# Kernel tuning notes

Hardware: AMD Instinct MI355X
Metric: run time of the kernel (lower is better)

The kernel has to match this reference:

```python
import jax, jax.numpy as jnp
import numpy as np
from jax import lax

EPS = 1e-5
ODE_T1 = 6.0      # ODEnet uses timestep=6
ODE_NSTEPS = 12   # fixed-step RK4 replacing scipy LSODA


def _gn(x, groups, w, b):
    # GroupNorm over (C//groups, H, W) per group, affine per-channel
    N, C, H, W = x.shape
    xg = x.reshape(N, groups, -1)
    mu = xg.mean(-1, keepdims=True)
    var = xg.var(-1, keepdims=True)
    xn = ((xg - mu) * lax.rsqrt(var + EPS)).reshape(N, C, H, W)
    return xn * w[None, :, None, None] + b[None, :, None, None]


def _conv(x, w, stride=1, pad=1):
    return lax.conv_general_dilated(
        x, w, (stride, stride), [(pad, pad), (pad, pad)],
        dimension_numbers=('NCHW', 'OIHW', 'NCHW'))


def _residual(x, g1w, g1b, c1w, g2w, g2b, c2w, dw):
    # Residual block with stride-2 conv and 1x1 stride-2 downsample applied
    # to relu(norm1(x)) (exactly as in the torch code).
    h = jax.nn.relu(_gn(x, 32, g1w, g1b))
    skip = _conv(h, dw, stride=2, pad=0)
    h = _conv(h, c1w, stride=2, pad=1)
    h = jax.nn.relu(_gn(h, 32, g2w, g2b))
    h = _conv(h, c2w)
    return h + skip


def _odefunc(z, p):
    # ResidualODE.odefunc: GroupNorm with groups == channels (64)
    g1w, g1b, c1w, g2w, g2b, c2w = p
    h = jax.nn.relu(_gn(z, 64, g1w, g1b))
    h = _conv(h, c1w)
    h = jax.nn.relu(_gn(h, 64, g2w, g2b))
    h = _conv(h, c2w)
    return h + z


def _odeint_rk4(z0, p):
    dt = ODE_T1 / ODE_NSTEPS
    def step(z, _):
        k1 = _odefunc(z, p)
        k2 = _odefunc(z + 0.5 * dt * k1, p)
        k3 = _odefunc(z + 0.5 * dt * k2, p)
        k4 = _odefunc(z + dt * k3, p)
        return z + (dt / 6.0) * (k1 + 2.0 * k2 + 2.0 * k3 + k4), None
    z, _ = lax.scan(step, z0, None, length=ODE_NSTEPS)
    return z


def _forward(x, conv1_w, conv1_b,
             r1_g1w, r1_g1b, r1_c1w, r1_g2w, r1_g2b, r1_c2w, r1_dw,
             r2_g1w, r2_g1b, r2_c1w, r2_g2w, r2_g2b, r2_c2w, r2_dw,
             ode_g1w, ode_g1b, ode_c1w, ode_g2w, ode_g2b, ode_c2w,
             fin_gw, fin_gb, fc_w, fc_b):
    out = _conv(x, conv1_w, stride=1, pad=0) + conv1_b[None, :, None, None]  # (B,64,26,26)
    out = _residual(out, r1_g1w, r1_g1b, r1_c1w, r1_g2w, r1_g2b, r1_c2w, r1_dw)  # (B,64,13,13)
    out = _residual(out, r2_g1w, r2_g1b, r2_c1w, r2_g2w, r2_g2b, r2_c2w, r2_dw)  # (B,64,7,7)
    out = _odeint_rk4(out, (ode_g1w, ode_g1b, ode_c1w, ode_g2w, ode_g2b, ode_c2w))
    out = jax.nn.relu(_gn(out, 32, fin_gw, fin_gb))
    out = out.mean(axis=(2, 3))  # AdaptiveAvgPool2d((1,1)) + flatten -> (B,64)
    return out @ fc_w.T + fc_b   # (B,10)


def setup_inputs() -> dict:
    key = jax.random.key(0)
    ks = iter(jax.random.split(key, 16))
    n = lambda shape, s: jax.random.normal(next(ks), shape, dtype=jnp.float32) * s
    C = 64
    s3 = 0.05  # ~ kaiming std for 64x3x3 fan-in
    inp = {
        'x': n((512, 1, 28, 28), 1.0),
        'conv1_w': n((C, 1, 3, 3), 0.3),
        'conv1_b': jnp.zeros((C,), jnp.float32),
        'r1_g1w': jnp.ones((C,), jnp.float32), 'r1_g1b': jnp.zeros((C,), jnp.float32),
        'r1_c1w': n((C, C, 3, 3), s3),
        'r1_g2w': jnp.ones((C,), jnp.float32), 'r1_g2b': jnp.zeros((C,), jnp.float32),
        'r1_c2w': n((C, C, 3, 3), s3),
        'r1_dw': n((C, C, 1, 1), 0.12),
        'r2_g1w': jnp.ones((C,), jnp.float32), 'r2_g1b': jnp.zeros((C,), jnp.float32),
        'r2_c1w': n((C, C, 3, 3), s3),
        'r2_g2w': jnp.ones((C,), jnp.float32), 'r2_g2b': jnp.zeros((C,), jnp.float32),
        'r2_c2w': n((C, C, 3, 3), s3),
        'r2_dw': n((C, C, 1, 1), 0.12),
        'ode_g1w': jnp.ones((C,), jnp.float32), 'ode_g1b': jnp.zeros((C,), jnp.float32),
        'ode_c1w': n((C, C, 3, 3), s3),
        'ode_g2w': jnp.ones((C,), jnp.float32), 'ode_g2b': jnp.zeros((C,), jnp.float32),
        'ode_c2w': n((C, C, 3, 3), s3),
        'fin_gw': jnp.ones((C,), jnp.float32), 'fin_gb': jnp.zeros((C,), jnp.float32),
        'fc_w': n((10, C), 0.1),
        'fc_b': jnp.zeros((10,), jnp.float32),
    }
    return inp


def reference(x, conv1_w, conv1_b,
              r1_g1w, r1_g1b, r1_c1w, r1_g2w, r1_g2b, r1_c2w, r1_dw,
              r2_g1w, r2_g1b, r2_c1w, r2_g2w, r2_g2b, r2_c2w, r2_dw,
              ode_g1w, ode_g1b, ode_c1w, ode_g2w, ode_g2b, ode_c2w,
              fin_gw, fin_gb, fc_w, fc_b):
    return _forward(x, conv1_w, conv1_b,
                    r1_g1w, r1_g1b, r1_c1w, r1_g2w, r1_g2b, r1_c2w, r1_dw,
                    r2_g1w, r2_g1b, r2_c1w, r2_g2w, r2_g2b, r2_c2w, r2_dw,
                    ode_g1w, ode_g1b, ode_c1w, ode_g2w, ode_g2b, ode_c2w,
                    fin_gw, fin_gb, fc_w, fc_b)
```

## Files before the change

### kernel.cpp

```cpp
#include <hip/hip_runtime.h>
#include <hip/hip_bf16.h>

#define TPB 256

typedef __attribute__((ext_vector_type(8))) short short8;
typedef __attribute__((ext_vector_type(4))) float f32x4;

__device__ __forceinline__ unsigned short f2bf(float x) {
    union { float f; unsigned int u; } c; c.f = x;
    unsigned int u = c.u;
    unsigned int r = (u + 0x7fffu + ((u >> 16) & 1u)) >> 16;
    return (unsigned short)r;
}


__global__ void conv1_k(const float* __restrict__ x, const float* __restrict__ w,
                        const float* __restrict__ b, float* __restrict__ out) {
    int idx = blockIdx.x * TPB + threadIdx.x;
    const int total = 512 * 64 * 26 * 26;
    if (idx >= total) return;
    int ox = idx % 26; int t = idx / 26;
    int oy = t % 26;   t /= 26;
    int co = t % 64;   int n = t / 64;
    const float* xp = x + (size_t)n * 784 + oy * 28 + ox;
    const float* wp = w + co * 9;
    float s = b[co];
#pragma unroll
    for (int ky = 0; ky < 3; ky++)
#pragma unroll
        for (int kx = 0; kx < 3; kx++)
            s += xp[ky * 28 + kx] * wp[ky * 3 + kx];
    out[idx] = s;
}

__global__ void gn_stats_k(const float* __restrict__ x, float* __restrict__ mean,
                           float* __restrict__ rstd, int N, int C, int HW, int G) {
    int gid  = (blockIdx.x * blockDim.x + threadIdx.x) >> 6;
    int lane = threadIdx.x & 63;
    int total = N * G;
    if (gid >= total) return;
    int n = gid / G, g = gid % G;
    int cpg = C / G;
    int gsize = cpg * HW;
    const float* p = x + ((size_t)n * C + (size_t)g * cpg) * HW;
    float s = 0.f, s2 = 0.f;
    for (int i = lane; i < gsize; i += 64) { float v = p[i]; s += v; s2 += v * v; }
#pragma unroll
    for (int off = 32; off; off >>= 1) {
        s  += __shfl_down(s,  off);
        s2 += __shfl_down(s2, off);
    }
    if (lane == 0) {
        float m = s / gsize;
        float var = s2 / gsize - m * m;
        mean[gid] = m;
        rstd[gid] = rsqrtf(var + 1e-5f);
    }
}

__global__ void wsplit_k(const float* __restrict__ w, unsigned short* __restrict__ hiT) {
    int i = blockIdx.x * TPB + threadIdx.x;
    if (i >= 9 * 2 * 4 * 64 * 8) return;
    int j = i & 7, l = (i >> 3) & 63, nt = (i >> 9) & 3, ks = (i >> 11) & 1, t = i >> 12;
    int co = nt * 16 + (l & 15);
    int ci = ks * 32 + (l >> 4) * 8 + j;
    hiT[i] = f2bf(w[(co * 64 + ci) * 9 + t]);
}

__global__ void wsplit1_k(const float* __restrict__ w, unsigned short* __restrict__ hiT) {
    int i = blockIdx.x * TPB + threadIdx.x;
    if (i >= 2 * 4 * 64 * 8) return;
    int j = i & 7, l = (i >> 3) & 63, nt = (i >> 9) & 3, ks = (i >> 11) & 1;
    int co = nt * 16 + (l & 15);
    int ci = ks * 32 + (l >> 4) * 8 + j;
    hiT[i] = f2bf(w[co * 64 + ci]);
}


__global__ __launch_bounds__(256, 2)
void conv_s2_mfma_k(const float* __restrict__ in,
                    const unsigned short* __restrict__ bhT,
                    const unsigned short* __restrict__ dwT,
                    float* __restrict__ out, float* __restrict__ skipout,
                    const float* __restrict__ mean, const float* __restrict__ rstd,
                    const float* __restrict__ gnw, const float* __restrict__ gnb,
                    int H, int W, int OH, int OW, int TX, int TY) {
    __shared__ unsigned short hp[256 * 72];

    int b = blockIdx.x;
    int tx = b % TX; b /= TX;
    int ty = b % TY; int n = b / TY;
    int oy0 = ty * 7, ox0 = tx * 7;

    const int t = threadIdx.x;
    const int lane = t & 63, nt = t >> 6;
    const int colL = lane & 15, q = lane >> 4;
    const int co = nt * 16 + colL;
    const int kq0 = q * 8;

    short8 wr[18], dr[2];
#pragma unroll
    for (int i = 0; i < 18; i++) wr[i] = ((const short8*)bhT)[(i * 4 + nt) * 64 + lane];
    dr[0] = ((const short8*)dwT)[(0 * 4 + nt) * 64 + lane];
    dr[1] = ((const short8*)dwT)[(1 * 4 + nt) * 64 + lane];

    for (int i = t; i < 256 * 72 / 2; i += 256) ((unsigned int*)hp)[i] = 0u;
    __syncthreads();

    const float* ip = in + (size_t)n * 64 * H * W;
    for (int i = t; i < 64 * 240; i += 256) {
        int ch = i / 240; int rc = i - ch * 240;
        int r = rc >> 4, c = rc & 15;
        int iy = 2 * oy0 - 1 + r;
        int ix = (c < 8) ? (2 * ox0 + 2 * c) : (2 * ox0 - 1 + 2 * (c - 8));
        if ((unsigned)iy < (unsigned)H && (unsigned)ix < (unsigned)W) {
            float m = mean[n * 32 + (ch >> 1)], rs = rstd[n * 32 + (ch >> 1)];
            float raw = ip[(size_t)ch * H * W + iy * W + ix];
            float v = fmaxf((raw - m) * rs * gnw[ch] + gnb[ch], 0.f);
            hp[(r * 16 + c) * 72 + ch] = f2bf(v);
        }
    }
    __syncthreads();

    int bs0, bs1, bs2, bs3;
    {
#define BSLOT(dst, mm)                                                          \
        {                                                                       \
            int p_ = (mm) * 16 + colL;                                          \
            int oy_ = p_ >> 3, ox_ = p_ & 7;                                    \
            dst = (ox_ < 7 && oy_ < 7) ? ((2 * oy_) * 16 + ox_) : 0;            \
        }
        BSLOT(bs0, 0) BSLOT(bs1, 1) BSLOT(bs2, 2) BSLOT(bs3, 3)
#undef BSLOT
    }

    f32x4 a0, a1, a2, a3, k0, k1, k2, k3;
    a0 = (f32x4){0.f, 0.f, 0.f, 0.f}; a1 = a0; a2 = a0; a3 = a0;
    k0 = a0; k1 = a0; k2 = a0; k3 = a0;

#pragma unroll
    for (int t9 = 0; t9 < 9; t9++) {
        const int kx = t9 % 3;
        const int toff = (t9 / 3) * 16 + (kx == 0 ? 8 : (kx == 1 ? 0 : 9));
#pragma unroll
        for (int ks = 0; ks < 2; ks++) {
            short8 vb = wr[t9 * 2 + ks];
            int kq = ks * 32 + kq0;
#define TAP(areg, bs)                                                           \
            {                                                                   \
                short8 av = *(const short8*)(hp + ((bs) + toff) * 72 + kq);     \
                areg = __builtin_amdgcn_mfma_f32_16x16x32_bf16(av, vb, areg, 0, 0, 0); \
            }
            TAP(a0, bs0) TAP(a1, bs1) TAP(a2, bs2) TAP(a3, bs3)
#undef TAP
        }
    }
#pragma unroll
    for (int ks = 0; ks < 2; ks++) {
        short8 vb = dr[ks];
        int kq = ks * 32 + kq0;
#define TAP(areg, bs)                                                           \
        {                                                                       \
            short8 av = *(const short8*)(hp + ((bs) + 16) * 72 + kq);           \
            areg = __builtin_amdgcn_mfma_f32_16x16x32_bf16(av, vb, areg, 0, 0, 0); \
        }
        TAP(k0, bs0) TAP(k1, bs1) TAP(k2, bs2) TAP(k3, bs3)
#undef TAP
    }

#define WB(areg, kreg, mm)                                                      \
    _Pragma("unroll")                                                           \
    for (int j = 0; j < 4; j++) {                                               \
        int p_ = (mm) * 16 + q * 4 + j;                                         \
        int oy_ = p_ >> 3, ox_ = p_ & 7;                                        \
        if (ox_ < 7 && oy_ < 7 && oy0 + oy_ < OH && ox0 + ox_ < OW) {           \
            size_t idx = (((size_t)n * 64 + co) * OH + oy0 + oy_) * OW + ox0 + ox_; \
            out[idx] = areg[j];                                                 \
            skipout[idx] = kreg[j];                                             \
        }                                                                       \
    }
    WB(a0, k0, 0) WB(a1, k1, 1) WB(a2, k2, 2) WB(a3, k3, 3)
#undef WB
}


__global__ __launch_bounds__(256, 2)
void conv13_mfma_k(const float* __restrict__ in, const unsigned short* __restrict__ bhT,
                   float* __restrict__ io,
                   const float* __restrict__ mean, const float* __restrict__ rstd,
                   const float* __restrict__ gnw, const float* __restrict__ gnb) {
    __shared__ unsigned short hp[256 * 72];
    const int t = threadIdx.x;
    const int n = blockIdx.x;
    const int lane = t & 63;
    const int nt = t >> 6;
    const int colL = lane & 15, q = lane >> 4;
    const int co = nt * 16 + colL;
    const int kq0 = q * 8;

    short8 wr[18];
#pragma unroll
    for (int i = 0; i < 18; i++) wr[i] = ((const short8*)bhT)[(i * 4 + nt) * 64 + lane];

    for (int i = t; i < 256 * 72 / 2; i += 256) ((unsigned int*)hp)[i] = 0u;
    __syncthreads();
    const float* ip = in + (size_t)n * 64 * 169;
    for (int i = t; i < 64 * 169; i += 256) {
        int ch = i / 169, p = i - ch * 169;
        int y = p / 13, x = p - y * 13;
        float m = mean[n * 32 + (ch >> 1)], rs = rstd[n * 32 + (ch >> 1)];
        float v = fmaxf((ip[i] - m) * rs * gnw[ch] + gnb[ch], 0.f);
        hp[((y + 1) * 16 + (x + 1)) * 72 + ch] = f2bf(v);
    }
    __syncthreads();

    int hb[11];
#pragma unroll
    for (int m = 0; m < 11; m++) {
        int p = m * 16 + colL;
        int y = p / 13, x = p - y * 13;
        hb[m] = (y + 1) * 16 + (x + 1);
    }
    f32x4 acc[11];
#pragma unroll
    for (int m = 0; m < 11; m++) acc[m] = (f32x4){0.f, 0.f, 0.f, 0.f};

#pragma unroll
    for (int t9 = 0; t9 < 9; t9++) {
        const int toff = (t9 / 3) * 16 + (t9 % 3) - 17;
#pragma unroll
        for (int ks = 0; ks < 2; ks++) {
            short8 vb = wr[t9 * 2 + ks];
            int kq = ks * 32 + kq0;
#pragma unroll
            for (int m = 0; m < 11; m++) {
                short8 a_ = *(const short8*)(hp + (hb[m] + toff) * 72 + kq);
                acc[m] = __builtin_amdgcn_mfma_f32_16x16x32_bf16(a_, vb, acc[m], 0, 0, 0);
            }
        }
    }

    float* op = io + (size_t)n * 64 * 169 + (size_t)co * 169;
#pragma unroll
    for (int m = 0; m < 11; m++) {
        int p0 = m * 16 + q * 4;
#pragma unroll
        for (int j = 0; j < 4; j++) {
            int p = p0 + j;
            if (p < 169) op[p] += acc[m][j];
        }
    }
}


#define HP_PITCH 72
#define HP_PLANE (100 * HP_PITCH)

#define PVALID(p) ((((p) & 7) < 7) && (((p) >> 3) < 7))
#define PSLOT(p)  (((((p) >> 3) + 1) * 10) + (((p) & 7) + 1))

#define CONV_TAP(areg, hbase)                                                   \
    {                                                                           \
        short8 a_ = *(const short8*)(hp + ((hbase) + toff) * HP_PITCH + kq);    \
        areg = __builtin_amdgcn_mfma_f32_16x16x32_bf16(a_, vb, areg, 0, 0, 0);  \
    }

#define CONV_MFMA(hpsrc, wreg)                                                  \
    a0 = (f32x4){0.f, 0.f, 0.f, 0.f}; a1 = a0; a2 = a0; a3 = a0;                \
    {                                                                           \
        const unsigned short* hp = (hpsrc);                                     \
        _Pragma("unroll")                                                       \
        for (int t9 = 0; t9 < 9; t9++) {                                        \
            const int toff = (t9 / 3) * 10 + (t9 % 3) - 11;                     \
            _Pragma("unroll")                                                   \
            for (int ks = 0; ks < 2; ks++) {                                    \
                short8 vb = wreg[t9 * 2 + ks];                                  \
                int kq = ks * 32 + kq0;                                         \
                CONV_TAP(a0, h0)                                                \
                CONV_TAP(a1, h1)                                                \
                CONV_TAP(a2, h2)                                                \
                CONV_TAP(a3, h3)                                                \
            }                                                                   \
        }                                                                       \
    }

#define CONV_MFMA_G(hpsrc, bhT)                                                 \
    a0 = (f32x4){0.f, 0.f, 0.f, 0.f}; a1 = a0; a2 = a0; a3 = a0;                \
    {                                                                           \
        const unsigned short* hp = (hpsrc);                                     \
        const short8* bh_ = (const short8*)(bhT);                               \
        _Pragma("unroll")                                                       \
        for (int t9 = 0; t9 < 9; t9++) {                                        \
            const int toff = (t9 / 3) * 10 + (t9 % 3) - 11;                     \
            _Pragma("unroll")                                                   \
            for (int ks = 0; ks < 2; ks++) {                                    \
                short8 vb = bh_[((t9 * 2 + ks) * 4 + nt) * 64 + lane];          \
                int kq = ks * 32 + kq0;                                         \
                CONV_TAP(a0, h0)                                                \
                CONV_TAP(a1, h1)                                                \
                CONV_TAP(a2, h2)                                                \
                CONV_TAP(a3, h3)                                                \
            }                                                                   \
        }                                                                       \
    }

#define GN_ACCUM(areg, mm)                                                      \
    _Pragma("unroll")                                                           \
    for (int j = 0; j < 4; j++) {                                               \
        int p_ = (mm) * 16 + q * 4 + j;                                         \
        if (PVALID(p_)) { float x_ = areg[j]; s += x_; s2 += x_ * x_; }         \
    }

#define GN_STORE(dst, areg, mm)                                                 \
    _Pragma("unroll")                                                           \
    for (int j = 0; j < 4; j++) {                                               \
        int p_ = (mm) * 16 + q * 4 + j;                                         \
        if (PVALID(p_)) {                                                       \
            float y_ = fmaxf(areg[j] * sc + sh, 0.f);                           \
            (dst)[PSLOT(p_) * HP_PITCH + co] = f2bf(y_);                        \
        }                                                                       \
    }

#define RK4_REG(areg, zm, zam, um)                                              \
    {                                                                           \
        f32x4 kv = areg + um;                                                   \
        zam = (e == 0) ? (zm + ck * kv) : (zam + ck * kv);                      \
        if (e < 3) um = zm + cu * kv;                                           \
    }

__global__ __launch_bounds__(256, 2)
void ode_mfma_k(const float* __restrict__ u7raw, const float* __restrict__ z7,
                const float* __restrict__ mean, const float* __restrict__ rstd,
                const float* __restrict__ pgw, const float* __restrict__ pgb,
                const unsigned short* __restrict__ wr2h,
                const unsigned short* __restrict__ wb1h,
                const unsigned short* __restrict__ wb2h,
                const float* __restrict__ g1w, const float* __restrict__ g1b,
                const float* __restrict__ g2w, const float* __restrict__ g2b,
                const float* __restrict__ fgw, const float* __restrict__ fgb,
                const float* __restrict__ fcw, const float* __restrict__ fcb,
                float* __restrict__ out) {
    __shared__ unsigned short hp1[HP_PLANE], hp2[HP_PLANE];
    __shared__ float pooled[64];

    const int t = threadIdx.x;
    const int n = blockIdx.x;
    const int lane = t & 63;
    const int nt = t >> 6;
    const int colL = lane & 15, q = lane >> 4;
    const int co = nt * 16 + colL;

    const float g1wv = g1w[co], g1bv = g1b[co];
    const float g2wv = g2w[co], g2bv = g2b[co];

    const int h0 = PSLOT(colL);
    const int h1 = PSLOT(16 + colL);
    const int h2 = PSLOT(32 + colL);
    const int h3 = PSLOT(48 + colL);
    const int kq0 = q * 8;

    short8 w1r[18], w2r[18];
#pragma unroll
    for (int i = 0; i < 18; i++) {
        int fidx = (i * 4 + nt) * 64 + lane;
        w1r[i] = ((const short8*)wb1h)[fidx];
        w2r[i] = ((const short8*)wb2h)[fidx];
    }

    for (int i = t; i < HP_PLANE; i += 256) { hp1[i] = 0; hp2[i] = 0; }
    __syncthreads();

    {
        const float* up = u7raw + (size_t)n * 3136;
        for (int i = t; i < 3136; i += 256) {
            int ch = i / 49, r = i - ch * 49;
            int y = r / 7, x = r - y * 7;
            float m = mean[n * 32 + (ch >> 1)], rs = rstd[n * 32 + (ch >> 1)];
            float v = fmaxf((up[i] - m) * rs * pgw[ch] + pgb[ch], 0.f);
            hp1[((y + 1) * 10 + (x + 1)) * HP_PITCH + ch] = f2bf(v);
        }
    }
    __syncthreads();

    f32x4 zr0, zr1, zr2, zr3;
    f32x4 za0, za1, za2, za3;
    f32x4 ur0, ur1, ur2, ur3;
    {
        f32x4 a0, a1, a2, a3;
        CONV_MFMA_G(hp1, wr2h)
        const float* zb = z7 + (size_t)n * 3136 + (size_t)co * 49;
#define INITZ(zm, areg, mm)                                                     \
        _Pragma("unroll")                                                       \
        for (int j = 0; j < 4; j++) {                                           \
            int p_ = (mm) * 16 + q * 4 + j;                                     \
            zm[j] = PVALID(p_) ? (areg[j] + zb[(p_ >> 3) * 7 + (p_ & 7)]) : 0.f;\
        }
        INITZ(zr0, a0, 0) INITZ(zr1, a1, 1) INITZ(zr2, a2, 2) INITZ(zr3, a3, 3)
#undef INITZ
    }
    ur0 = zr0; ur1 = zr1; ur2 = zr2; ur3 = zr3;
    __syncthreads();

    const float dt = 0.5f;

#pragma unroll 1
    for (int step = 0; step < 12; step++) {
#pragma unroll 1
        for (int e = 0; e < 4; e++) {
            const float ck = (e == 0 || e == 3) ? dt / 6.f : dt / 3.f;
            const float cu = (e == 2) ? dt : 0.5f * dt;

            {
                float s = 0.f, s2 = 0.f;
                GN_ACCUM(ur0, 0) GN_ACCUM(ur1, 1) GN_ACCUM(ur2, 2) GN_ACCUM(ur3, 3)
                s += __shfl_xor(s, 16); s2 += __shfl_xor(s2, 16);
                s += __shfl_xor(s, 32); s2 += __shfl_xor(s2, 32);
                float mu = s * (1.f / 49.f);
                float r = rsqrtf(s2 * (1.f / 49.f) - mu * mu + 1e-5f);
                float sc = r * g1wv, sh = g1bv - mu * sc;
                GN_STORE(hp1, ur0, 0) GN_STORE(hp1, ur1, 1)
                GN_STORE(hp1, ur2, 2) GN_STORE(hp1, ur3, 3)
            }
            __syncthreads();

            {
                f32x4 a0, a1, a2, a3;
                CONV_MFMA(hp1, w1r)

                float s = 0.f, s2 = 0.f;
                GN_ACCUM(a0, 0) GN_ACCUM(a1, 1) GN_ACCUM(a2, 2) GN_ACCUM(a3, 3)
                s += __shfl_xor(s, 16); s2 += __shfl_xor(s2, 16);
                s += __shfl_xor(s, 32); s2 += __shfl_xor(s2, 32);
                float mu = s * (1.f / 49.f);
                float r = rsqrtf(s2 * (1.f / 49.f) - mu * mu + 1e-5f);
                float sc = r * g2wv, sh = g2bv - mu * sc;
                GN_STORE(hp2, a0, 0) GN_STORE(hp2, a1, 1)
                GN_STORE(hp2, a2, 2) GN_STORE(hp2, a3, 3)
            }
            __syncthreads();

            {
                f32x4 a0, a1, a2, a3;
                CONV_MFMA(hp2, w2r)

                RK4_REG(a0, zr0, za0, ur0) RK4_REG(a1, zr1, za1, ur1)
                RK4_REG(a2, zr2, za2, ur2) RK4_REG(a3, zr3, za3, ur3)
                if (e == 3) {
                    zr0 = za0; zr1 = za1; zr2 = za2; zr3 = za3;
                    ur0 = zr0; ur1 = zr1; ur2 = zr2; ur3 = zr3;
                }
            }
        }
    }

    {
        float s = 0.f, s2 = 0.f;
        GN_ACCUM(zr0, 0) GN_ACCUM(zr1, 1) GN_ACCUM(zr2, 2) GN_ACCUM(zr3, 3)
        s += __shfl_xor(s, 16); s2 += __shfl_xor(s2, 16);
        s += __shfl_xor(s, 32); s2 += __shfl_xor(s2, 32);
        s += __shfl_xor(s, 1);  s2 += __shfl_xor(s2, 1);
        float mu = s * (1.f / 98.f);
        float r = rsqrtf(s2 * (1.f / 98.f) - mu * mu + 1e-5f);
        float sc = r * fgw[co], sh = fgb[co] - mu * sc;
        float ps = 0.f;
#pragma unroll
        for (int mm = 0; mm < 4; mm++) {
            f32x4 zz = (mm == 0) ? zr0 : (mm == 1) ? zr1 : (mm == 2) ? zr2 : zr3;
#pragma unroll
            for (int j = 0; j < 4; j++) {
                int p_ = mm * 16 + q * 4 + j;
                if (PVALID(p_)) ps += fmaxf(zz[j] * sc + sh, 0.f);
            }
        }
        ps += __shfl_xor(ps, 16);
        ps += __shfl_xor(ps, 32);
        if (q == 0) pooled[co] = ps * (1.f / 49.f);
    }
    __syncthreads();
    if (t < 10) {
        float a = fcb[t];
#pragma unroll
        for (int k = 0; k < 64; k++) a += pooled[k] * fcw[t * 64 + k];
        out[(size_t)n * 10 + t] = a;
    }
}

static inline int nblk(long long total) { return (int)((total + TPB - 1) / TPB); }

extern "C" void kernel_launch(void* const* d_in, const int* in_sizes, int n_in,
                              void* d_out, int out_size, void* d_ws, size_t ws_size,
                              hipStream_t stream) {
    const float* x       = (const float*)d_in[0];
    const float* conv1_w = (const float*)d_in[1];
    const float* conv1_b = (const float*)d_in[2];
    const float* r1_g1w  = (const float*)d_in[3];
    const float* r1_g1b  = (const float*)d_in[4];
    const float* r1_c1w  = (const float*)d_in[5];
    const float* r1_g2w  = (const float*)d_in[6];
    const float* r1_g2b  = (const float*)d_in[7];
    const float* r1_c2w  = (const float*)d_in[8];
    const float* r1_dw   = (const float*)d_in[9];
    const float* r2_g1w  = (const float*)d_in[10];
    const float* r2_g1b  = (const float*)d_in[11];
    const float* r2_c1w  = (const float*)d_in[12];
    const float* r2_g2w  = (const float*)d_in[13];
    const float* r2_g2b  = (const float*)d_in[14];
    const float* r2_c2w  = (const float*)d_in[15];
    const float* r2_dw   = (const float*)d_in[16];
    const float* o_g1w   = (const float*)d_in[17];
    const float* o_g1b   = (const float*)d_in[18];
    const float* o_c1w   = (const float*)d_in[19];
    const float* o_g2w   = (const float*)d_in[20];
    const float* o_g2b   = (const float*)d_in[21];
    const float* o_c2w   = (const float*)d_in[22];
    const float* fin_gw  = (const float*)d_in[23];
    const float* fin_gb  = (const float*)d_in[24];
    const float* fc_w    = (const float*)d_in[25];
    const float* fc_b    = (const float*)d_in[26];
    float* out = (float*)d_out;

    const int N = 512;
    const long long SZ26 = 512LL * 64 * 26 * 26;
    const long long SZ13 = 512LL * 64 * 13 * 13;
    const long long SZ7  = 512LL * 64 * 7 * 7;
    const long long WBS  = 9 * 2 * 4 * 64 * 8;
    const long long WBS1 = 2 * 4 * 64 * 8;

    float* B26   = (float*)d_ws;
    float* A13   = B26 + SZ26;
    float* B13   = A13 + SZ13;
    float* Z7    = B13 + SZ13;
    float* U7    = Z7 + SZ7;
    float* MEAN  = U7 + SZ7;
    float* RSTD  = MEAN + 512 * 32;
    unsigned short* WB1h  = (unsigned short*)(RSTD + 512 * 32);
    unsigned short* WB2h  = WB1h + WBS;
    unsigned short* WB13h = WB2h + WBS;
    unsigned short* WR2h  = WB13h + WBS;
    unsigned short* WR11h = WR2h + WBS;
    unsigned short* WR21h = WR11h + WBS;
    unsigned short* WD1h  = WR21h + WBS;
    unsigned short* WD2h  = WD1h + WBS1;

    wsplit_k<<<nblk(WBS), TPB, 0, stream>>>(o_c1w, WB1h);
    wsplit_k<<<nblk(WBS), TPB, 0, stream>>>(o_c2w, WB2h);
    wsplit_k<<<nblk(WBS), TPB, 0, stream>>>(r1_c2w, WB13h);
    wsplit_k<<<nblk(WBS), TPB, 0, stream>>>(r2_c2w, WR2h);
    wsplit_k<<<nblk(WBS), TPB, 0, stream>>>(r1_c1w, WR11h);
    wsplit_k<<<nblk(WBS), TPB, 0, stream>>>(r2_c1w, WR21h);
    wsplit1_k<<<nblk(WBS1), TPB, 0, stream>>>(r1_dw, WD1h);
    wsplit1_k<<<nblk(WBS1), TPB, 0, stream>>>(r2_dw, WD2h);

    conv1_k<<<nblk(SZ26), TPB, 0, stream>>>(x, conv1_w, conv1_b, B26);

    gn_stats_k<<<nblk(512LL * 32 * 64), TPB, 0, stream>>>(B26, MEAN, RSTD, N, 64, 676, 32);
    conv_s2_mfma_k<<<512 * 4, 256, 0, stream>>>(B26, WR11h, WD1h, A13, B13,
                                                MEAN, RSTD, r1_g1w, r1_g1b,
                                                26, 26, 13, 13, 2, 2);
    gn_stats_k<<<nblk(512LL * 32 * 64), TPB, 0, stream>>>(A13, MEAN, RSTD, N, 64, 169, 32);
    conv13_mfma_k<<<512, 256, 0, stream>>>(A13, WB13h, B13, MEAN, RSTD, r1_g2w, r1_g2b);

    gn_stats_k<<<nblk(512LL * 32 * 64), TPB, 0, stream>>>(B13, MEAN, RSTD, N, 64, 169, 32);
    conv_s2_mfma_k<<<512, 256, 0, stream>>>(B13, WR21h, WD2h, U7, Z7,
                                            MEAN, RSTD, r2_g1w, r2_g1b,
                                            13, 13, 7, 7, 1, 1);
    gn_stats_k<<<nblk(512LL * 32 * 64), TPB, 0, stream>>>(U7, MEAN, RSTD, N, 64, 49, 32);

    ode_mfma_k<<<512, 256, 0, stream>>>(U7, Z7, MEAN, RSTD, r2_g2w, r2_g2b,
                                        WR2h, WB1h, WB2h,
                                        o_g1w, o_g1b, o_g2w, o_g2b,
                                        fin_gw, fin_gb, fc_w, fc_b, out);
}
```

Baseline: 632.6 us.

## Fuse GroupNorm statistics into consumer conv kernels and merge weight-split launches

Drops the four standalone gn_stats kernels. Each consumer kernel (strided conv, 13x13 conv, ODE kernel) now computes per-sample group mean and rstd itself with a shared-memory reduction before normalizing its input. The eight weight-conversion launches are also merged into one kernel. This removes several launches and a global round trip for the statistics. In exchange, the first strided conv recomputes the full-sample statistics in each of its four tile blocks, reading the whole 26x26 input four times.

```diff
diff --git a/kernel.cpp b/kernel.cpp
--- a/kernel.cpp
+++ b/kernel.cpp
@@ -12,6 +12,30 @@
     unsigned int r = (u + 0x7fffu + ((u >> 16) & 1u)) >> 16;
     return (unsigned short)r;
 }
+
+#define IN_STATS(Xp, HW)                                                        \
+    {                                                                           \
+        int ch_ = t >> 2, sg_ = t & 3;                                          \
+        float s_ = 0.f, s2_ = 0.f;                                              \
+        for (int i_ = sg_; i_ < (HW); i_ += 4) {                                \
+            float v_ = (Xp)[(size_t)ch_ * (HW) + i_];                           \
+            s_ += v_; s2_ += v_ * v_;                                           \
+        }                                                                       \
+        rsum[t] = s_; rssq[t] = s2_;                                            \
+        __syncthreads();                                                        \
+        if (t < 32) {                                                           \
+            float S = 0.f, S2 = 0.f;                                            \
+            _Pragma("unroll")                                                   \
+            for (int k_ = 0; k_ < 8; k_++) {                                    \
+                int tt_ = (2 * t + (k_ & 1)) * 4 + (k_ >> 1);                   \
+                S += rsum[tt_]; S2 += rssq[tt_];                                \
+            }                                                                   \
+            float mu_ = S / (2.f * (HW));                                       \
+            sM[t] = mu_;                                                        \
+            sR[t] = rsqrtf(S2 / (2.f * (HW)) - mu_ * mu_ + 1e-5f);              \
+        }                                                                       \
+        __syncthreads();                                                        \
+    }
 
 
 __global__ void conv1_k(const float* __restrict__ x, const float* __restrict__ w,
@@ -33,47 +57,32 @@
     out[idx] = s;
 }
 
-__global__ void gn_stats_k(const float* __restrict__ x, float* __restrict__ mean,
-                           float* __restrict__ rstd, int N, int C, int HW, int G) {
-    int gid  = (blockIdx.x * blockDim.x + threadIdx.x) >> 6;
-    int lane = threadIdx.x & 63;
-    int total = N * G;
-    if (gid >= total) return;
-    int n = gid / G, g = gid % G;
-    int cpg = C / G;
-    int gsize = cpg * HW;
-    const float* p = x + ((size_t)n * C + (size_t)g * cpg) * HW;
-    float s = 0.f, s2 = 0.f;
-    for (int i = lane; i < gsize; i += 64) { float v = p[i]; s += v; s2 += v * v; }
-#pragma unroll
-    for (int off = 32; off; off >>= 1) {
-        s  += __shfl_down(s,  off);
-        s2 += __shfl_down(s2, off);
-    }
-    if (lane == 0) {
-        float m = s / gsize;
-        float var = s2 / gsize - m * m;
-        mean[gid] = m;
-        rstd[gid] = rsqrtf(var + 1e-5f);
-    }
-}
-
-__global__ void wsplit_k(const float* __restrict__ w, unsigned short* __restrict__ hiT) {
+
+__global__ void wsplit_all_k(const float* __restrict__ w0, const float* __restrict__ w1,
+                             const float* __restrict__ w2, const float* __restrict__ w3,
+                             const float* __restrict__ w4, const float* __restrict__ w5,
+                             const float* __restrict__ d0, const float* __restrict__ d1,
+                             unsigned short* __restrict__ dst) {
+    const int WBS = 9 * 2 * 4 * 64 * 8, WBS1 = 2 * 4 * 64 * 8;
     int i = blockIdx.x * TPB + threadIdx.x;
-    if (i >= 9 * 2 * 4 * 64 * 8) return;
-    int j = i & 7, l = (i >> 3) & 63, nt = (i >> 9) & 3, ks = (i >> 11) & 1, t = i >> 12;
-    int co = nt * 16 + (l & 15);
-    int ci = ks * 32 + (l >> 4) * 8 + j;
-    hiT[i] = f2bf(w[(co * 64 + ci) * 9 + t]);
-}
-
-__global__ void wsplit1_k(const float* __restrict__ w, unsigned short* __restrict__ hiT) {
-    int i = blockIdx.x * TPB + threadIdx.x;
-    if (i >= 2 * 4 * 64 * 8) return;
-    int j = i & 7, l = (i >> 3) & 63, nt = (i >> 9) & 3, ks = (i >> 11) & 1;
-    int co = nt * 16 + (l & 15);
-    int ci = ks * 32 + (l >> 4) * 8 + j;
-    hiT[i] = f2bf(w[co * 64 + ci]);
+    if (i < 6 * WBS) {
+        int tbl = i / WBS; int r = i - tbl * WBS;
+        const float* w = (tbl == 0) ? w0 : (tbl == 1) ? w1 : (tbl == 2) ? w2
+                       : (tbl == 3) ? w3 : (tbl == 4) ? w4 : w5;
+        int j = r & 7, l = (r >> 3) & 63, nt = (r >> 9) & 3, ks = (r >> 11) & 1, tt = r >> 12;
+        int co = nt * 16 + (l & 15);
+        int ci = ks * 32 + (l >> 4) * 8 + j;
+        dst[i] = f2bf(w[(co * 64 + ci) * 9 + tt]);
+    } else {
+        int r = i - 6 * WBS;
+        if (r >= 2 * WBS1) return;
+        int tbl = r / WBS1; r -= tbl * WBS1;
+        const float* w = tbl ? d1 : d0;
+        int j = r & 7, l = (r >> 3) & 63, nt = (r >> 9) & 3, ks = (r >> 11) & 1;
+        int co = nt * 16 + (l & 15);
+        int ci = ks * 32 + (l >> 4) * 8 + j;
+        dst[6 * WBS + tbl * WBS1 + r] = f2bf(w[co * 64 + ci]);
+    }
 }
 
 
@@ -82,10 +91,10 @@
                     const unsigned short* __restrict__ bhT,
                     const unsigned short* __restrict__ dwT,
                     float* __restrict__ out, float* __restrict__ skipout,
-                    const float* __restrict__ mean, const float* __restrict__ rstd,
                     const float* __restrict__ gnw, const float* __restrict__ gnb,
                     int H, int W, int OH, int OW, int TX, int TY) {
     __shared__ unsigned short hp[256 * 72];
+    __shared__ float rsum[256], rssq[256], sM[32], sR[32];
 
     int b = blockIdx.x;
     int tx = b % TX; b /= TX;
@@ -105,16 +114,17 @@
     dr[1] = ((const short8*)dwT)[(1 * 4 + nt) * 64 + lane];
 
     for (int i = t; i < 256 * 72 / 2; i += 256) ((unsigned int*)hp)[i] = 0u;
-    __syncthreads();
 
     const float* ip = in + (size_t)n * 64 * H * W;
+    IN_STATS(ip, H * W)
+
     for (int i = t; i < 64 * 240; i += 256) {
         int ch = i / 240; int rc = i - ch * 240;
         int r = rc >> 4, c = rc & 15;
         int iy = 2 * oy0 - 1 + r;
         int ix = (c < 8) ? (2 * ox0 + 2 * c) : (2 * ox0 - 1 + 2 * (c - 8));
         if ((unsigned)iy < (unsigned)H && (unsigned)ix < (unsigned)W) {
-            float m = mean[n * 32 + (ch >> 1)], rs = rstd[n * 32 + (ch >> 1)];
+            float m = sM[ch >> 1], rs = sR[ch >> 1];
             float raw = ip[(size_t)ch * H * W + iy * W + ix];
             float v = fmaxf((raw - m) * rs * gnw[ch] + gnb[ch], 0.f);
             hp[(r * 16 + c) * 72 + ch] = f2bf(v);
@@ -187,9 +197,9 @@
 __global__ __launch_bounds__(256, 2)
 void conv13_mfma_k(const float* __restrict__ in, const unsigned short* __restrict__ bhT,
                    float* __restrict__ io,
-                   const float* __restrict__ mean, const float* __restrict__ rstd,
                    const float* __restrict__ gnw, const float* __restrict__ gnb) {
     __shared__ unsigned short hp[256 * 72];
+    __shared__ float rsum[256], rssq[256], sM[32], sR[32];
     const int t = threadIdx.x;
     const int n = blockIdx.x;
     const int lane = t & 63;
@@ -203,12 +213,14 @@
     for (int i = 0; i < 18; i++) wr[i] = ((const short8*)bhT)[(i * 4 + nt) * 64 + lane];
 
     for (int i = t; i < 256 * 72 / 2; i += 256) ((unsigned int*)hp)[i] = 0u;
-    __syncthreads();
+
     const float* ip = in + (size_t)n * 64 * 169;
+    IN_STATS(ip, 169)
+
     for (int i = t; i < 64 * 169; i += 256) {
         int ch = i / 169, p = i - ch * 169;
         int y = p / 13, x = p - y * 13;
-        float m = mean[n * 32 + (ch >> 1)], rs = rstd[n * 32 + (ch >> 1)];
+        float m = sM[ch >> 1], rs = sR[ch >> 1];
         float v = fmaxf((ip[i] - m) * rs * gnw[ch] + gnb[ch], 0.f);
         hp[((y + 1) * 16 + (x + 1)) * 72 + ch] = f2bf(v);
     }
@@ -330,7 +342,6 @@
 
 __global__ __launch_bounds__(256, 2)
 void ode_mfma_k(const float* __restrict__ u7raw, const float* __restrict__ z7,
-                const float* __restrict__ mean, const float* __restrict__ rstd,
                 const float* __restrict__ pgw, const float* __restrict__ pgb,
                 const unsigned short* __restrict__ wr2h,
                 const unsigned short* __restrict__ wb1h,
@@ -341,6 +352,7 @@
                 const float* __restrict__ fcw, const float* __restrict__ fcb,
                 float* __restrict__ out) {
     __shared__ unsigned short hp1[HP_PLANE], hp2[HP_PLANE];
+    __shared__ float rsum[256], rssq[256], sM[32], sR[32];
     __shared__ float pooled[64];
 
     const int t = threadIdx.x;
@@ -368,17 +380,16 @@
     }
 
     for (int i = t; i < HP_PLANE; i += 256) { hp1[i] = 0; hp2[i] = 0; }
-    __syncthreads();
-
-    {
-        const float* up = u7raw + (size_t)n * 3136;
-        for (int i = t; i < 3136; i += 256) {
-            int ch = i / 49, r = i - ch * 49;
-            int y = r / 7, x = r - y * 7;
-            float m = mean[n * 32 + (ch >> 1)], rs = rstd[n * 32 + (ch >> 1)];
-            float v = fmaxf((up[i] - m) * rs * pgw[ch] + pgb[ch], 0.f);
-            hp1[((y + 1) * 10 + (x + 1)) * HP_PITCH + ch] = f2bf(v);
-        }
+
+    const float* up = u7raw + (size_t)n * 3136;
+    IN_STATS(up, 49)
+
+    for (int i = t; i < 3136; i += 256) {
+        int ch = i / 49, r = i - ch * 49;
+        int y = r / 7, x = r - y * 7;
+        float m = sM[ch >> 1], rs = sR[ch >> 1];
+        float v = fmaxf((up[i] - m) * rs * pgw[ch] + pgb[ch], 0.f);
+        hp1[((y + 1) * 10 + (x + 1)) * HP_PITCH + ch] = f2bf(v);
     }
     __syncthreads();
 
@@ -519,7 +530,6 @@
     const float* fc_b    = (const float*)d_in[26];
     float* out = (float*)d_out;
 
-    const int N = 512;
     const long long SZ26 = 512LL * 64 * 26 * 26;
     const long long SZ13 = 512LL * 64 * 13 * 13;
     const long long SZ7  = 512LL * 64 * 7 * 7;
@@ -531,42 +541,29 @@
     float* B13   = A13 + SZ13;
     float* Z7    = B13 + SZ13;
     float* U7    = Z7 + SZ7;
-    float* MEAN  = U7 + SZ7;
-    float* RSTD  = MEAN + 512 * 32;
-    unsigned short* WB1h  = (unsigned short*)(RSTD + 512 * 32);
-    unsigned short* WB2h  = WB1h + WBS;
-    unsigned short* WB13h = WB2h + WBS;
-    unsigned short* WR2h  = WB13h + WBS;
-    unsigned short* WR11h = WR2h + WBS;
-    unsigned short* WR21h = WR11h + WBS;
-    unsigned short* WD1h  = WR21h + WBS;
-    unsigned short* WD2h  = WD1h + WBS1;
-
-    wsplit_k<<<nblk(WBS), TPB, 0, stream>>>(o_c1w, WB1h);
-    wsplit_k<<<nblk(WBS), TPB, 0, stream>>>(o_c2w, WB2h);
-    wsplit_k<<<nblk(WBS), TPB, 0, stream>>>(r1_c2w, WB13h);
-    wsplit_k<<<nblk(WBS), TPB, 0, stream>>>(r2_c2w, WR2h);
-    wsplit_k<<<nblk(WBS), TPB, 0, stream>>>(r1_c1w, WR11h);
-    wsplit_k<<<nblk(WBS), TPB, 0, stream>>>(r2_c1w, WR21h);
-    wsplit1_k<<<nblk(WBS1), TPB, 0, stream>>>(r1_dw, WD1h);
-    wsplit1_k<<<nblk(WBS1), TPB, 0, stream>>>(r2_dw, WD2h);
+    unsigned short* WTAB  = (unsigned short*)(U7 + SZ7);
+    unsigned short* WB1h  = WTAB;
+    unsigned short* WB2h  = WTAB + WBS;
+    unsigned short* WB13h = WTAB + 2 * WBS;
+    unsigned short* WR2h  = WTAB + 3 * WBS;
+    unsigned short* WR11h = WTAB + 4 * WBS;
+    unsigned short* WR21h = WTAB + 5 * WBS;
+    unsigned short* WD1h  = WTAB + 6 * WBS;
+    unsigned short* WD2h  = WTAB + 6 * WBS + WBS1;
+
+    wsplit_all_k<<<nblk(6 * WBS + 2 * WBS1), TPB, 0, stream>>>(
+        o_c1w, o_c2w, r1_c2w, r2_c2w, r1_c1w, r2_c1w, r1_dw, r2_dw, WTAB);
 
     conv1_k<<<nblk(SZ26), TPB, 0, stream>>>(x, conv1_w, conv1_b, B26);
 
-    gn_stats_k<<<nblk(512LL * 32 * 64), TPB, 0, stream>>>(B26, MEAN, RSTD, N, 64, 676, 32);
     conv_s2_mfma_k<<<512 * 4, 256, 0, stream>>>(B26, WR11h, WD1h, A13, B13,
-                                                MEAN, RSTD, r1_g1w, r1_g1b,
-                                                26, 26, 13, 13, 2, 2);
-    gn_stats_k<<<nblk(512LL * 32 * 64), TPB, 0, stream>>>(A13, MEAN, RSTD, N, 64, 169, 32);
-    conv13_mfma_k<<<512, 256, 0, stream>>>(A13, WB13h, B13, MEAN, RSTD, r1_g2w, r1_g2b);
-
-    gn_stats_k<<<nblk(512LL * 32 * 64), TPB, 0, stream>>>(B13, MEAN, RSTD, N, 64, 169, 32);
+                                                r1_g1w, r1_g1b, 26, 26, 13, 13, 2, 2);
+    conv13_mfma_k<<<512, 256, 0, stream>>>(A13, WB13h, B13, r1_g2w, r1_g2b);
+
     conv_s2_mfma_k<<<512, 256, 0, stream>>>(B13, WR21h, WD2h, U7, Z7,
-                                            MEAN, RSTD, r2_g1w, r2_g1b,
-                                            13, 13, 7, 7, 1, 1);
-    gn_stats_k<<<nblk(512LL * 32 * 64), TPB, 0, stream>>>(U7, MEAN, RSTD, N, 64, 49, 32);
-
-    ode_mfma_k<<<512, 256, 0, stream>>>(U7, Z7, MEAN, RSTD, r2_g2w, r2_g2b,
+                                            r2_g1w, r2_g1b, 13, 13, 7, 7, 1, 1);
+
+    ode_mfma_k<<<512, 256, 0, stream>>>(U7, Z7, r2_g2w, r2_g2b,
                                         WR2h, WB1h, WB2h,
                                         o_g1w, o_g1b, o_g2w, o_g2b,
                                         fin_gw, fin_gb, fc_w, fc_b, out);
```

Result: slower. 674.7 us (+6.7%).
